# Kernel optimization log

Hardware: AMD Instinct MI355X
Metric: run time of the kernel (lower is better)

The kernel has to match this reference:

```python
import jax, jax.numpy as jnp
from jax import lax
import numpy as np

N, E = 64, 126            # nodes per graph, directed edges (N = E//2 + 1)
BS, T = 32, 512           # batch, train_seq_len
G = BS * T                # total graphs
IN = N * 2                # encoder input_size
H8 = 128 * 8              # hidden_size * 8
OUT = 128                 # output_size (decoder GRU hidden)
L = 2                     # num_layers


def setup_inputs() -> dict:
    key = jax.random.key(0)
    ks = iter(jax.random.split(key, 64))
    def rn(shape, s=0.05):
        return jax.random.normal(next(ks), shape, dtype=jnp.float32) * s
    inp = {}
    inp['x'] = rn((G, N, 2), 1.0)
    inp['edge_index'] = jax.random.randint(next(ks), (2, E), 0, N)
    # GCN params (GCNConv(2,4), GCNConv(4,2), classifier Linear(2,2))
    inp['gcn_w1'] = rn((2, 4), 0.5); inp['gcn_b1'] = rn((4,))
    inp['gcn_w2'] = rn((4, 2), 0.5); inp['gcn_b2'] = rn((2,))
    inp['gcn_cw'] = rn((2, 2), 0.5); inp['gcn_cb'] = rn((2,))
    # Encoder: fl Linear(IN, H8); GRU(H8, H8, L)
    inp['enc_fl_w'] = rn((IN, H8)); inp['enc_fl_b'] = rn((H8,))
    inp['enc_wih'] = rn((L, 3 * H8, H8)); inp['enc_whh'] = rn((L, 3 * H8, H8))
    inp['enc_bih'] = rn((L, 3 * H8)); inp['enc_bhh'] = rn((L, 3 * H8))
    # Decoder: fl Linear(H8, H8); GRU(H8, OUT, L); Linear(OUT, OUT)
    inp['dec_fl_w'] = rn((H8, H8)); inp['dec_fl_b'] = rn((H8,))
    inp['dec_wih0'] = rn((3 * OUT, H8)); inp['dec_wih1'] = rn((3 * OUT, OUT))
    inp['dec_whh'] = rn((L, 3 * OUT, OUT))
    inp['dec_bih'] = rn((L, 3 * OUT)); inp['dec_bhh'] = rn((L, 3 * OUT))
    inp['dec_lin_w'] = rn((OUT, OUT)); inp['dec_lin_b'] = rn((OUT,))
    return inp


def _gcn_conv(h, src, dst, W, b):
    # PyG GCNConv: self-loops + symmetric normalization. h: [G, N, Fin]
    hw = h @ W                                   # [G, N, Fout]
    deg = jnp.ones((N,), hw.dtype).at[dst].add(jnp.ones((E,), hw.dtype))
    dinv = lax.rsqrt(deg)
    norm = dinv[src] * dinv[dst]                 # [E]
    msgs = hw[:, src, :] * norm[None, :, None]   # gather + scale
    agg = jnp.zeros_like(hw).at[:, dst, :].add(msgs)
    agg = agg + hw * (dinv * dinv)[None, :, None]  # self-loop term (norm = 1/deg)
    return agg + b


def _gru_layer(x_seq, wih, whh, bih, bhh):
    # x_seq: [B, T, D]; torch nn.GRU math, h0 = 0
    B = x_seq.shape[0]
    H = whh.shape[1]
    h0 = jnp.zeros((B, H), x_seq.dtype)
    def step(h, x_t):
        gi = x_t @ wih.T + bih
        gh = h @ whh.T + bhh
        i_r, i_z, i_n = jnp.split(gi, 3, axis=-1)
        h_r, h_z, h_n = jnp.split(gh, 3, axis=-1)
        r = jax.nn.sigmoid(i_r + h_r)
        z = jax.nn.sigmoid(i_z + h_z)
        n = jnp.tanh(i_n + r * h_n)
        h_new = (1.0 - z) * n + z * h
        return h_new, h_new
    _, ys = lax.scan(step, h0, jnp.swapaxes(x_seq, 0, 1))
    return jnp.swapaxes(ys, 0, 1)


def reference(x, edge_index, gcn_w1, gcn_b1, gcn_w2, gcn_b2, gcn_cw, gcn_cb,
              enc_fl_w, enc_fl_b, enc_wih, enc_whh, enc_bih, enc_bhh,
              dec_fl_w, dec_fl_b, dec_wih0, dec_wih1, dec_whh, dec_bih, dec_bhh,
              dec_lin_w, dec_lin_b):
    src, dst = edge_index[0], edge_index[1]
    # GCN over all G graphs at once (vectorizes the per-graph Python loop)
    h = jnp.tanh(_gcn_conv(x, src, dst, gcn_w1, gcn_b1))
    h = jnp.tanh(_gcn_conv(h, src, dst, gcn_w2, gcn_b2))
    h = h @ gcn_cw + gcn_cb                      # [G, N, 2]
    res = h.reshape(BS, T, IN)
    # Encoder
    out = jax.nn.relu(res @ enc_fl_w + enc_fl_b)
    for l in range(L):
        out = _gru_layer(out, enc_wih[l], enc_whh[l], enc_bih[l], enc_bhh[l])
    # Decoder (dropout in eval mode = identity)
    d = jax.nn.relu(out @ dec_fl_w + dec_fl_b)
    d = _gru_layer(d, dec_wih0, dec_whh[0], dec_bih[0], dec_bhh[0])
    d = _gru_layer(d, dec_wih1, dec_whh[1], dec_bih[1], dec_bhh[1])
    return d @ dec_lin_w + dec_lin_b             # [BS, T, OUT]
```

## Files before the change

kernel.cpp:

```cpp
#include <hip/hip_runtime.h>

typedef unsigned short u16;
typedef unsigned long long u64;
typedef __attribute__((ext_vector_type(8))) short bf16x8;
typedef __attribute__((ext_vector_type(4))) float f32x4;

#define BSZ 32
#define TT 512
#define GG (BSZ*TT)
#define NNODE 64
#define EE 126
#define H8 1024
#define H3 3072
#define NWAVE 128

__device__ __forceinline__ float b2f(u16 u){
  union { unsigned i; float f; } v; v.i = ((unsigned)u) << 16; return v.f;
}
__device__ __forceinline__ u16 f2b(float f){
  unsigned i = __float_as_uint(f);
  unsigned r = (i + 0x7FFFu + ((i >> 16) & 1u)) >> 16;
  return (u16)r;
}
__device__ __forceinline__ float sigm(float x){ return 1.f/(1.f+__expf(-x)); }
__device__ __forceinline__ float tanh_f(float x){
  float xc = fminf(fmaxf(x, -15.f), 15.f);
  float e = __expf(2.f*xc);
  return (e-1.f)/(e+1.f);
}
__device__ __forceinline__ int prow(int m, int perm){
  return perm ? ((m & (TT-1))*BSZ + (m >> 9)) : m;
}

__global__ __launch_bounds__(256) void detect_dtype(const void* xraw, int* flag){
  __shared__ int cnt;
  if (threadIdx.x == 0) cnt = 0;
  __syncthreads();
  const u16* p = (const u16*)xraw;
  u16 u = p[2*threadIdx.x];
  int e = (u >> 7) & 0xFF;
  int weird = (e < 100 || e > 134) ? 1 : 0;
  atomicAdd(&cnt, weird);
  __syncthreads();
  if (threadIdx.x == 0) *flag = (cnt > 128) ? 1 : 0;
}

__global__ __launch_bounds__(256) void cvt_bf16(const void* __restrict__ in,
                                                u16* __restrict__ out, int n,
                                                const int* __restrict__ flag){
  int i = blockIdx.x*256 + threadIdx.x;
  if (i >= n) return;
  if (*flag) out[i] = f2b(((const float*)in)[i]);
  else       out[i] = ((const u16*)in)[i];
}

__global__ __launch_bounds__(64) void gcn_kernel(
    const u16* __restrict__ x, const int* __restrict__ ei,
    const u16* __restrict__ w1, const u16* __restrict__ b1,
    const u16* __restrict__ w2, const u16* __restrict__ b2,
    const u16* __restrict__ cw, const u16* __restrict__ cb,
    u16* __restrict__ res)
{
  __shared__ int se[EE], de[EE];
  __shared__ float dinv[NNODE];
  __shared__ float nrm[EE];
  __shared__ float hs[NNODE][4];
  const int n = threadIdx.x;
  const int g = blockIdx.x;
  for (int e = n; e < EE; e += 64){ se[e] = ei[e]; de[e] = ei[EE + e]; }
  __syncthreads();
  int cnt = 0;
  for (int e = 0; e < EE; e++) cnt += (de[e] == n) ? 1 : 0;
  float di = rsqrtf(1.0f + (float)cnt);
  dinv[n] = di;
  float x0 = b2f(x[((size_t)g*NNODE + n)*2 + 0]);
  float x1 = b2f(x[((size_t)g*NNODE + n)*2 + 1]);
  float hw[4];
  #pragma unroll
  for (int c = 0; c < 4; c++) hw[c] = x0*b2f(w1[c]) + x1*b2f(w1[4+c]);
  #pragma unroll
  for (int c = 0; c < 4; c++) hs[n][c] = hw[c];
  __syncthreads();
  for (int e = n; e < EE; e += 64) nrm[e] = dinv[se[e]] * dinv[de[e]];
  __syncthreads();
  float selfc = di*di;
  float agg[4];
  #pragma unroll
  for (int c = 0; c < 4; c++) agg[c] = hw[c]*selfc;
  for (int e = 0; e < EE; e++){
    if (de[e] == n){
      float w = nrm[e]; int s = se[e];
      #pragma unroll
      for (int c = 0; c < 4; c++) agg[c] += hs[s][c]*w;
    }
  }
  float h1[4];
  #pragma unroll
  for (int c = 0; c < 4; c++) h1[c] = tanh_f(agg[c] + b2f(b1[c]));
  __syncthreads();
  float hw2[2];
  #pragma unroll
  for (int c = 0; c < 2; c++){
    float s = 0.f;
    #pragma unroll
    for (int k = 0; k < 4; k++) s += h1[k]*b2f(w2[k*2+c]);
    hw2[c] = s;
    hs[n][c] = s;
  }
  __syncthreads();
  float agg2[2] = { hw2[0]*selfc, hw2[1]*selfc };
  for (int e = 0; e < EE; e++){
    if (de[e] == n){
      float w = nrm[e]; int s = se[e];
      agg2[0] += hs[s][0]*w;
      agg2[1] += hs[s][1]*w;
    }
  }
  float h2a = tanh_f(agg2[0] + b2f(b2[0]));
  float h2b = tanh_f(agg2[1] + b2f(b2[1]));
  #pragma unroll
  for (int c = 0; c < 2; c++){
    float o = h2a*b2f(cw[c]) + h2b*b2f(cw[2+c]) + b2f(cb[c]);
    res[(size_t)g*128 + n*2 + c] = f2b(o);
  }
}

__global__ __launch_bounds__(256) void transpose_bf16(
    const u16* __restrict__ in, u16* __restrict__ out, int R, int C)
{
  __shared__ u16 tile[32][33];
  int c0 = blockIdx.x*32, r0 = blockIdx.y*32;
  for (int i = threadIdx.y; i < 32; i += 8)
    tile[i][threadIdx.x] = in[(size_t)(r0+i)*C + c0 + threadIdx.x];
  __syncthreads();
  for (int i = threadIdx.y; i < 32; i += 8)
    out[(size_t)(c0+i)*R + r0 + threadIdx.x] = tile[threadIdx.x][i];
}

__global__ __launch_bounds__(256) void gemm_nt(
    const u16* __restrict__ A, const u16* __restrict__ Bm,
    const u16* __restrict__ bias, void* __restrict__ C,
    int M, int N, int K, int relu, int permA, int permC,
    const int* __restrict__ outflag)
{
  const int wave = threadIdx.x >> 6;
  const int lane = threadIdx.x & 63;
  const int wm = wave >> 1, wn = wave & 1;
  const int q = lane >> 4, lr = lane & 15;
  const int mBase = blockIdx.y*128 + wm*64;
  const int nBase = blockIdx.x*128 + wn*64;
  f32x4 acc[4][4] = {};
  const u16* ap[4]; const u16* bp[4];
  #pragma unroll
  for (int i = 0; i < 4; i++){
    ap[i] = A + (size_t)prow(mBase + i*16 + lr, permA)*K + q*8;
    bp[i] = Bm + (size_t)(nBase + i*16 + lr)*K + q*8;
  }
  for (int kb = 0; kb < K; kb += 32){
    bf16x8 av[4], bv[4];
    #pragma unroll
    for (int i = 0; i < 4; i++){
      av[i] = *(const bf16x8*)ap[i]; bv[i] = *(const bf16x8*)bp[i];
      ap[i] += 32; bp[i] += 32;
    }
    #pragma unroll
    for (int mi = 0; mi < 4; mi++)
      #pragma unroll
      for (int ni = 0; ni < 4; ni++)
        acc[mi][ni] = __builtin_amdgcn_mfma_f32_16x16x32_bf16(av[mi], bv[ni], acc[mi][ni], 0, 0, 0);
  }
  const int of32 = outflag ? *outflag : 0;
  #pragma unroll
  for (int ni = 0; ni < 4; ni++){
    int col = nBase + ni*16 + lr;
    float bb = bias ? b2f(bias[col]) : 0.f;
    #pragma unroll
    for (int mi = 0; mi < 4; mi++){
      #pragma unroll
      for (int r = 0; r < 4; r++){
        int row = prow(mBase + mi*16 + q*4 + r, permC);
        float v = acc[mi][ni][r] + bb;
        if (relu) v = fmaxf(v, 0.f);
        size_t idx = (size_t)row*N + col;
        if (of32) ((float*)C)[idx] = v;
        else      ((u16*)C)[idx]   = f2b(v);
      }
    }
  }
}

__global__ __launch_bounds__(64) void enc_rec(
    const u16* __restrict__ gi,
    const u16* __restrict__ whh,
    const u16* __restrict__ bhh,
    u16* __restrict__ seq,
    int* __restrict__ cnt)
{
  const int wg = blockIdx.x;
  const int lane = threadIdx.x & 63;
  const int q = lane >> 4, lr = lane & 15;
  const int j = (wg >> 1)*16 + lr;
  const int bbase = (wg & 1)*16;
  const int sub = wg & 7;
  const float bh_r = b2f(bhh[j]);
  const float bh_z = b2f(bhh[H8 + j]);
  const float bh_n = b2f(bhh[2*H8 + j]);
  const u16* wp0 = whh + (size_t)(0*H8 + j)*H8 + q*8;
  const u16* wp1 = whh + (size_t)(1*H8 + j)*H8 + q*8;
  const u16* wp2 = whh + (size_t)(2*H8 + j)*H8 + q*8;
  float hreg[4] = {0.f,0.f,0.f,0.f};
  u16 gpre[12];
  #pragma unroll
  for (int r = 0; r < 4; r++){
    size_t row = (size_t)(bbase + q*4 + r)*H3;
    gpre[r]   = gi[row + j];
    gpre[4+r] = gi[row + H8 + j];
    gpre[8+r] = gi[row + 2*H8 + j];
  }
  for (int t = 0; t < TT; t++){
    if (t > 0){
      for (;;){
        int s = 0;
        #pragma unroll
        for (int i = 0; i < 8; i++)
          s += __hip_atomic_load(&cnt[i*TT + (t-1)], __ATOMIC_RELAXED, __HIP_MEMORY_SCOPE_AGENT);
        if (s == NWAVE) break;
        __builtin_amdgcn_s_sleep(1);
      }
      asm volatile("" ::: "memory");
    }
    float gr_[4], gz_[4], gn_[4];
    #pragma unroll
    for (int r = 0; r < 4; r++){
      gr_[r] = b2f(gpre[r]); gz_[r] = b2f(gpre[4+r]); gn_[r] = b2f(gpre[8+r]);
    }
    f32x4 acc0 = {}, acc1 = {}, acc2 = {};
    if (t > 0){
      const u16* ap = seq + (size_t)((t-1)*BSZ + bbase + lr)*H8 + q*8;
      #pragma unroll 8
      for (int kb = 0; kb < 32; kb++){
        const u64* p = (const u64*)(ap + kb*32);
        u64 lo = __hip_atomic_load(p,     __ATOMIC_RELAXED, __HIP_MEMORY_SCOPE_AGENT);
        u64 hi = __hip_atomic_load(p + 1, __ATOMIC_RELAXED, __HIP_MEMORY_SCOPE_AGENT);
        union { u64 v[2]; bf16x8 b; } a; a.v[0] = lo; a.v[1] = hi;
        bf16x8 w0 = *(const bf16x8*)(wp0 + kb*32);
        bf16x8 w1 = *(const bf16x8*)(wp1 + kb*32);
        bf16x8 w2 = *(const bf16x8*)(wp2 + kb*32);
        acc0 = __builtin_amdgcn_mfma_f32_16x16x32_bf16(a.b, w0, acc0, 0,0,0);
        acc1 = __builtin_amdgcn_mfma_f32_16x16x32_bf16(a.b, w1, acc1, 0,0,0);
        acc2 = __builtin_amdgcn_mfma_f32_16x16x32_bf16(a.b, w2, acc2, 0,0,0);
      }
    }
    #pragma unroll
    for (int r = 0; r < 4; r++){
      float rr = sigm(gr_[r] + acc0[r] + bh_r);
      float zz = sigm(gz_[r] + acc1[r] + bh_z);
      float nn = tanh_f(gn_[r] + rr*(acc2[r] + bh_n));
      float hnew = (1.f - zz)*nn + zz*hreg[r];
      hreg[r] = hnew;
      __hip_atomic_store(&seq[(size_t)(t*BSZ + bbase + q*4 + r)*H8 + j], f2b(hnew),
                         __ATOMIC_RELAXED, __HIP_MEMORY_SCOPE_AGENT);
    }
    asm volatile("s_waitcnt vmcnt(0)" ::: "memory");
    if (lane == 0)
      __hip_atomic_fetch_add(&cnt[sub*TT + t], 1, __ATOMIC_RELAXED, __HIP_MEMORY_SCOPE_AGENT);
    if (t + 1 < TT){
      #pragma unroll
      for (int r = 0; r < 4; r++){
        size_t row = (size_t)((t+1)*BSZ + bbase + q*4 + r)*H3;
        gpre[r]   = gi[row + j];
        gpre[4+r] = gi[row + H8 + j];
        gpre[8+r] = gi[row + 2*H8 + j];
      }
    }
  }
}

__global__ __launch_bounds__(256) void dec_rec(
    const u16* __restrict__ gi,
    const u16* __restrict__ whh,
    const u16* __restrict__ bhh,
    u16* __restrict__ seq)
{
  __shared__ u16 hlds[16*136];
  const int bb = blockIdx.x*16;
  const int tid = threadIdx.x;
  const int w = tid >> 6, lane = tid & 63, q = lane >> 4, lr = lane & 15;
  bf16x8 wreg[3][2][4];
  #pragma unroll
  for (int g2 = 0; g2 < 3; g2++)
    #pragma unroll
    for (int nt = 0; nt < 2; nt++){
      int jj = g2*128 + w*32 + nt*16 + lr;
      #pragma unroll
      for (int kb = 0; kb < 4; kb++)
        wreg[g2][nt][kb] = *(const bf16x8*)(whh + (size_t)jj*128 + kb*32 + q*8);
    }
  float bh[3][2];
  #pragma unroll
  for (int g2 = 0; g2 < 3; g2++)
    #pragma unroll
    for (int nt = 0; nt < 2; nt++)
      bh[g2][nt] = b2f(bhh[g2*128 + w*32 + nt*16 + lr]);
  float hreg[2][4] = {};
  u16 gpre[3][2][4];
  #pragma unroll
  for (int r = 0; r < 4; r++){
    size_t row = (size_t)(bb + q*4 + r)*384;
    #pragma unroll
    for (int nt = 0; nt < 2; nt++){
      int jj = w*32 + nt*16 + lr;
      #pragma unroll
      for (int g2 = 0; g2 < 3; g2++)
        gpre[g2][nt][r] = gi[row + g2*128 + jj];
    }
  }
  __syncthreads();
  for (int t = 0; t < TT; t++){
    float gif[3][2][4];
    #pragma unroll
    for (int g2 = 0; g2 < 3; g2++)
      #pragma unroll
      for (int nt = 0; nt < 2; nt++)
        #pragma unroll
        for (int r = 0; r < 4; r++)
          gif[g2][nt][r] = b2f(gpre[g2][nt][r]);
    f32x4 acc[3][2] = {};
    if (t > 0){
      #pragma unroll
      for (int kb = 0; kb < 4; kb++){
        bf16x8 a = *(const bf16x8*)(hlds + lr*136 + kb*32 + q*8);
        #pragma unroll
        for (int g2 = 0; g2 < 3; g2++)
          #pragma unroll
          for (int nt = 0; nt < 2; nt++)
            acc[g2][nt] = __builtin_amdgcn_mfma_f32_16x16x32_bf16(a, wreg[g2][nt][kb], acc[g2][nt], 0,0,0);
      }
    }
    __syncthreads();
    #pragma unroll
    for (int nt = 0; nt < 2; nt++)
      #pragma unroll
      for (int r = 0; r < 4; r++){
        int jj = w*32 + nt*16 + lr;
        int b = bb + q*4 + r;
        float rr = sigm(gif[0][nt][r] + acc[0][nt][r] + bh[0][nt]);
        float zz = sigm(gif[1][nt][r] + acc[1][nt][r] + bh[1][nt]);
        float nn = tanh_f(gif[2][nt][r] + rr*(acc[2][nt][r] + bh[2][nt]));
        float hnew = (1.f - zz)*nn + zz*hreg[nt][r];
        hreg[nt][r] = hnew;
        u16 hb = f2b(hnew);
        hlds[(q*4 + r)*136 + jj] = hb;
        seq[(size_t)(t*BSZ + b)*128 + jj] = hb;
      }
    if (t + 1 < TT){
      #pragma unroll
      for (int r = 0; r < 4; r++){
        size_t row = (size_t)((t+1)*BSZ + bb + q*4 + r)*384;
        #pragma unroll
        for (int nt = 0; nt < 2; nt++){
          int jj = w*32 + nt*16 + lr;
          #pragma unroll
          for (int g2 = 0; g2 < 3; g2++)
            gpre[g2][nt][r] = gi[row + g2*128 + jj];
        }
      }
    }
    __syncthreads();
  }
}

extern "C" void kernel_launch(void* const* d_in, const int* in_sizes, int n_in,
                              void* d_out, int out_size, void* d_ws, size_t ws_size,
                              hipStream_t stream)
{
  const void* x    = d_in[0];
  const int* ei    = (const int*)d_in[1];

  const size_t NEED = (size_t)164 << 20;
  if (ws_size < NEED) return;
  char* wsb = (char*)d_ws;
  const size_t KB = 1024, MB = 1024*1024;

  int* syncv = (int*)wsb;
  int* flag  = (int*)(wsb + 40*KB);
  u16* gw1_c  = (u16*)(wsb + 1*MB + 0);
  u16* gb1_c  = (u16*)(wsb + 1*MB + 64);
  u16* gw2_c  = (u16*)(wsb + 1*MB + 128);
  u16* gb2_c  = (u16*)(wsb + 1*MB + 192);
  u16* gcw_c  = (u16*)(wsb + 1*MB + 256);
  u16* gcb_c  = (u16*)(wsb + 1*MB + 320);
  u16* efb_c  = (u16*)(wsb + 1*MB + 4*KB);
  u16* ebih_c = (u16*)(wsb + 1*MB + 8*KB);
  u16* ebhh_c = (u16*)(wsb + 1*MB + 24*KB);
  u16* dfb_c  = (u16*)(wsb + 1*MB + 40*KB);
  u16* dbih_c = (u16*)(wsb + 1*MB + 45*KB);
  u16* dbhh_c = (u16*)(wsb + 1*MB + 47*KB);
  u16* dlb_c  = (u16*)(wsb + 1*MB + 49*KB);
  u16* wT3    = (u16*)(wsb + 1*MB + 64*KB);
  u16* dlw_c  = (u16*)(wsb + 1*MB + 128*KB);
  u16* efw_c  = (u16*)(wsb + 1*MB + 192*KB);
  u16* wT1    = (u16*)(wsb + 1*MB + 448*KB);
  u16* dfw_c  = (u16*)(wsb + 2*MB);
  u16* wT2    = (u16*)(wsb + 4*MB);
  u16* dwih0_c= (u16*)(wsb + 6*MB);
  u16* dwih1_c= (u16*)(wsb + 7*MB);
  u16* dwhh_c = (u16*)(wsb + 7*MB + 128*KB);
  u16* ewih_c = (u16*)(wsb + 8*MB);
  u16* ewhh_c = (u16*)(wsb + 20*MB);
  u16* res    = (u16*)(wsb + 32*MB);
  u16* bufA   = (u16*)(wsb + 36*MB);
  u16* bufC   = (u16*)(wsb + 68*MB);
  u16* x_c    = bufC;
  u16* giD    = (u16*)(wsb + 100*MB);

  hipMemsetAsync(syncv, 0, 32*KB, stream);
  detect_dtype<<<1, 256, 0, stream>>>(x, flag);

  auto cvt = [&](int idx, u16* dst, int n){
    cvt_bf16<<<(n + 255)/256, 256, 0, stream>>>(d_in[idx], dst, n, flag);
  };
  cvt(0,  x_c,     GG*NNODE*2);
  cvt(2,  gw1_c, 8);  cvt(3, gb1_c, 4);  cvt(4, gw2_c, 8);
  cvt(5,  gb2_c, 2);  cvt(6, gcw_c, 4);  cvt(7, gcb_c, 2);
  cvt(8,  efw_c,   128*1024);   cvt(9,  efb_c, 1024);
  cvt(10, ewih_c,  2*3072*1024);
  cvt(11, ewhh_c,  2*3072*1024);
  cvt(12, ebih_c,  2*3072);     cvt(13, ebhh_c, 2*3072);
  cvt(14, dfw_c,   1024*1024);  cvt(15, dfb_c, 1024);
  cvt(16, dwih0_c, 384*1024);   cvt(17, dwih1_c, 384*128);
  cvt(18, dwhh_c,  2*384*128);
  cvt(19, dbih_c,  2*384);      cvt(20, dbhh_c, 2*384);
  cvt(21, dlw_c,   128*128);    cvt(22, dlb_c, 128);

  transpose_bf16<<<dim3(1024/32, 128/32),  dim3(32,8), 0, stream>>>(efw_c, wT1, 128, 1024);
  transpose_bf16<<<dim3(1024/32, 1024/32), dim3(32,8), 0, stream>>>(dfw_c, wT2, 1024, 1024);
  transpose_bf16<<<dim3(128/32, 128/32),   dim3(32,8), 0, stream>>>(dlw_c, wT3, 128, 128);

  gcn_kernel<<<GG, 64, 0, stream>>>(x_c, ei, gw1_c, gb1_c, gw2_c, gb2_c, gcw_c, gcb_c, res);

  gemm_nt<<<dim3(1024/128, GG/128), 256, 0, stream>>>(res, wT1, efb_c, bufA, GG, 1024, 128, 1, 0, 1, nullptr);
  gemm_nt<<<dim3(3072/128, GG/128), 256, 0, stream>>>(bufA, ewih_c, ebih_c, bufC, GG, 3072, 1024, 0, 1, 1, nullptr);
  enc_rec<<<NWAVE, 64, 0, stream>>>(bufC, ewhh_c, ebhh_c, bufA, syncv);
  gemm_nt<<<dim3(3072/128, GG/128), 256, 0, stream>>>(bufA, ewih_c + 3072*1024, ebih_c + 3072, bufC, GG, 3072, 1024, 0, 1, 1, nullptr);
  enc_rec<<<NWAVE, 64, 0, stream>>>(bufC, ewhh_c + 3072*1024, ebhh_c + 3072, bufA, syncv + 8*TT);

  u16* d0 = bufC;
  gemm_nt<<<dim3(1024/128, GG/128), 256, 0, stream>>>(bufA, wT2, dfb_c, d0, GG, 1024, 1024, 1, 1, 1, nullptr);
  gemm_nt<<<dim3(384/128, GG/128), 256, 0, stream>>>(d0, dwih0_c, dbih_c, giD, GG, 384, 1024, 0, 1, 1, nullptr);
  dec_rec<<<2, 256, 0, stream>>>(giD, dwhh_c, dbhh_c, res);
  gemm_nt<<<dim3(384/128, GG/128), 256, 0, stream>>>(res, dwih1_c, dbih_c + 384, giD, GG, 384, 128, 0, 1, 1, nullptr);
  dec_rec<<<2, 256, 0, stream>>>(giD, dwhh_c + 384*128, dbhh_c + 384, bufA);

  gemm_nt<<<dim3(128/128, GG/128), 256, 0, stream>>>(bufA, wT3, dlb_c, d_out, GG, 128, 128, 0, 1, 0, flag);
}
```

Before: 12.47 ms.

## Wavefront-pipeline encoder GRU layers and fuse decoder layers with output linear

Runs both encoder GRU layers in one persistent kernel, with layer 1 one step behind layer 0. Layer 1 computes its input projection on the fly from the layer-0 state instead of a separate full-sequence GEMM, and both layers share a global-counter barrier. The decoder's two GRU layers and the final linear are fused into one 512-thread block pipeline that uses double-buffered LDS states and prefetches the gate inputs. This removes two recurrent launches, one large GEMM and the serialized layer-1 time chain. In exchange, layer-1 waves do more per-step work, namely the input matmul streamed from global weights each step, and twice as many waves contend on the spin barrier.

```diff
diff --git a/kernel.cpp b/kernel.cpp
--- a/kernel.cpp
+++ b/kernel.cpp
@@ -12,7 +12,7 @@
 #define EE 126
 #define H8 1024
 #define H3 3072
-#define NWAVE 128
+#define NARRIVE 256
 
 __device__ __forceinline__ float b2f(u16 u){
   union { unsigned i; float f; } v; v.i = ((unsigned)u) << 16; return v.f;
@@ -30,6 +30,9 @@
 }
 __device__ __forceinline__ int prow(int m, int perm){
   return perm ? ((m & (TT-1))*BSZ + (m >> 9)) : m;
+}
+__device__ __forceinline__ u64 aload64(const u64* p){
+  return __hip_atomic_load(p, __ATOMIC_RELAXED, __HIP_MEMORY_SCOPE_AGENT);
 }
 
 __global__ __launch_bounds__(256) void detect_dtype(const void* xraw, int* flag){
@@ -139,9 +142,8 @@
 
 __global__ __launch_bounds__(256) void gemm_nt(
     const u16* __restrict__ A, const u16* __restrict__ Bm,
-    const u16* __restrict__ bias, void* __restrict__ C,
-    int M, int N, int K, int relu, int permA, int permC,
-    const int* __restrict__ outflag)
+    const u16* __restrict__ bias, u16* __restrict__ C,
+    int M, int N, int K, int relu, int permA, int permC)
 {
   const int wave = threadIdx.x >> 6;
   const int lane = threadIdx.x & 63;
@@ -169,7 +171,6 @@
       for (int ni = 0; ni < 4; ni++)
         acc[mi][ni] = __builtin_amdgcn_mfma_f32_16x16x32_bf16(av[mi], bv[ni], acc[mi][ni], 0, 0, 0);
   }
-  const int of32 = outflag ? *outflag : 0;
   #pragma unroll
   for (int ni = 0; ni < 4; ni++){
     int col = nBase + ni*16 + lr;
@@ -181,192 +182,337 @@
         int row = prow(mBase + mi*16 + q*4 + r, permC);
         float v = acc[mi][ni][r] + bb;
         if (relu) v = fmaxf(v, 0.f);
-        size_t idx = (size_t)row*N + col;
-        if (of32) ((float*)C)[idx] = v;
-        else      ((u16*)C)[idx]   = f2b(v);
+        C[(size_t)row*N + col] = f2b(v);
       }
     }
   }
 }
 
-__global__ __launch_bounds__(64) void enc_rec(
-    const u16* __restrict__ gi,
-    const u16* __restrict__ whh,
-    const u16* __restrict__ bhh,
-    u16* __restrict__ seq,
-    int* __restrict__ cnt)
+__device__ __forceinline__ void spinwait(int* cnt, int r){
+  for (;;){
+    int s = 0;
+    #pragma unroll
+    for (int i = 0; i < 8; i++)
+      s += __hip_atomic_load(&cnt[i*(TT+1) + r], __ATOMIC_RELAXED, __HIP_MEMORY_SCOPE_AGENT);
+    if (s == NARRIVE) break;
+    __builtin_amdgcn_s_sleep(1);
+  }
+  asm volatile("" ::: "memory");
+}
+
+__global__ __launch_bounds__(64) void enc_fused(
+    const u16* gi,
+    const u16* wih1,
+    const u16* whh0, const u16* whh1,
+    const u16* bih1, const u16* bhh0, const u16* bhh1,
+    u16* h0seq,
+    u16* h1seq,
+    int* cnt)
 {
-  const int wg = blockIdx.x;
+  const int wid = blockIdx.x;
+  const int stage = wid >> 7;
+  const int wid2 = wid & 127;
   const int lane = threadIdx.x & 63;
   const int q = lane >> 4, lr = lane & 15;
-  const int j = (wg >> 1)*16 + lr;
-  const int bbase = (wg & 1)*16;
-  const int sub = wg & 7;
-  const float bh_r = b2f(bhh[j]);
-  const float bh_z = b2f(bhh[H8 + j]);
-  const float bh_n = b2f(bhh[2*H8 + j]);
-  const u16* wp0 = whh + (size_t)(0*H8 + j)*H8 + q*8;
-  const u16* wp1 = whh + (size_t)(1*H8 + j)*H8 + q*8;
-  const u16* wp2 = whh + (size_t)(2*H8 + j)*H8 + q*8;
+  const int jg = wid2 >> 1, bh = wid2 & 1;
+  const int j = jg*16 + lr;
+  const int bbase = bh*16;
+  const int sub = wid & 7;
   float hreg[4] = {0.f,0.f,0.f,0.f};
-  u16 gpre[12];
-  #pragma unroll
-  for (int r = 0; r < 4; r++){
-    size_t row = (size_t)(bbase + q*4 + r)*H3;
-    gpre[r]   = gi[row + j];
-    gpre[4+r] = gi[row + H8 + j];
-    gpre[8+r] = gi[row + 2*H8 + j];
-  }
-  for (int t = 0; t < TT; t++){
-    if (t > 0){
-      for (;;){
-        int s = 0;
-        #pragma unroll
-        for (int i = 0; i < 8; i++)
-          s += __hip_atomic_load(&cnt[i*TT + (t-1)], __ATOMIC_RELAXED, __HIP_MEMORY_SCOPE_AGENT);
-        if (s == NWAVE) break;
-        __builtin_amdgcn_s_sleep(1);
+
+  if (stage == 0){
+    const float bh_r = b2f(bhh0[j]);
+    const float bh_z = b2f(bhh0[H8 + j]);
+    const float bh_n = b2f(bhh0[2*H8 + j]);
+    const u16* wp0 = whh0 + (size_t)(0*H8 + j)*H8 + q*8;
+    const u16* wp1 = whh0 + (size_t)(1*H8 + j)*H8 + q*8;
+    const u16* wp2 = whh0 + (size_t)(2*H8 + j)*H8 + q*8;
+    u16 gpre[12];
+    #pragma unroll
+    for (int r = 0; r < 4; r++){
+      size_t row = (size_t)(bbase + q*4 + r)*H3;
+      gpre[r]   = gi[row + j];
+      gpre[4+r] = gi[row + H8 + j];
+      gpre[8+r] = gi[row + 2*H8 + j];
+    }
+    for (int rd = 0; rd <= TT; rd++){
+      if (rd > 0) spinwait(cnt, rd - 1);
+      if (rd < TT){
+        const int t = rd;
+        float gr_[4], gz_[4], gn_[4];
+        #pragma unroll
+        for (int r = 0; r < 4; r++){
+          gr_[r] = b2f(gpre[r]); gz_[r] = b2f(gpre[4+r]); gn_[r] = b2f(gpre[8+r]);
+        }
+        f32x4 acc0 = {}, acc1 = {}, acc2 = {};
+        if (t > 0){
+          const u16* ap = h0seq + (size_t)((t-1)*BSZ + bbase + lr)*H8 + q*8;
+          #pragma unroll 8
+          for (int kb = 0; kb < 32; kb++){
+            const u64* p = (const u64*)(ap + kb*32);
+            union { u64 v[2]; bf16x8 b; } A; A.v[0] = aload64(p); A.v[1] = aload64(p+1);
+            bf16x8 w0 = *(const bf16x8*)(wp0 + kb*32);
+            bf16x8 w1 = *(const bf16x8*)(wp1 + kb*32);
+            bf16x8 w2 = *(const bf16x8*)(wp2 + kb*32);
+            acc0 = __builtin_amdgcn_mfma_f32_16x16x32_bf16(A.b, w0, acc0, 0,0,0);
+            acc1 = __builtin_amdgcn_mfma_f32_16x16x32_bf16(A.b, w1, acc1, 0,0,0);
+            acc2 = __builtin_amdgcn_mfma_f32_16x16x32_bf16(A.b, w2, acc2, 0,0,0);
+          }
+        }
+        #pragma unroll
+        for (int r = 0; r < 4; r++){
+          float rr = sigm(gr_[r] + acc0[r] + bh_r);
+          float zz = sigm(gz_[r] + acc1[r] + bh_z);
+          float nn = tanh_f(gn_[r] + rr*(acc2[r] + bh_n));
+          float hnew = (1.f - zz)*nn + zz*hreg[r];
+          hreg[r] = hnew;
+          __hip_atomic_store(&h0seq[(size_t)(t*BSZ + bbase + q*4 + r)*H8 + j], f2b(hnew),
+                             __ATOMIC_RELAXED, __HIP_MEMORY_SCOPE_AGENT);
+        }
       }
-      asm volatile("" ::: "memory");
-    }
-    float gr_[4], gz_[4], gn_[4];
-    #pragma unroll
-    for (int r = 0; r < 4; r++){
-      gr_[r] = b2f(gpre[r]); gz_[r] = b2f(gpre[4+r]); gn_[r] = b2f(gpre[8+r]);
-    }
-    f32x4 acc0 = {}, acc1 = {}, acc2 = {};
-    if (t > 0){
-      const u16* ap = seq + (size_t)((t-1)*BSZ + bbase + lr)*H8 + q*8;
-      #pragma unroll 8
-      for (int kb = 0; kb < 32; kb++){
-        const u64* p = (const u64*)(ap + kb*32);
-        u64 lo = __hip_atomic_load(p,     __ATOMIC_RELAXED, __HIP_MEMORY_SCOPE_AGENT);
-        u64 hi = __hip_atomic_load(p + 1, __ATOMIC_RELAXED, __HIP_MEMORY_SCOPE_AGENT);
-        union { u64 v[2]; bf16x8 b; } a; a.v[0] = lo; a.v[1] = hi;
-        bf16x8 w0 = *(const bf16x8*)(wp0 + kb*32);
-        bf16x8 w1 = *(const bf16x8*)(wp1 + kb*32);
-        bf16x8 w2 = *(const bf16x8*)(wp2 + kb*32);
-        acc0 = __builtin_amdgcn_mfma_f32_16x16x32_bf16(a.b, w0, acc0, 0,0,0);
-        acc1 = __builtin_amdgcn_mfma_f32_16x16x32_bf16(a.b, w1, acc1, 0,0,0);
-        acc2 = __builtin_amdgcn_mfma_f32_16x16x32_bf16(a.b, w2, acc2, 0,0,0);
+      asm volatile("s_waitcnt vmcnt(0)" ::: "memory");
+      if (lane == 0)
+        __hip_atomic_fetch_add(&cnt[sub*(TT+1) + rd], 1, __ATOMIC_RELAXED, __HIP_MEMORY_SCOPE_AGENT);
+      if (rd + 1 < TT){
+        #pragma unroll
+        for (int r = 0; r < 4; r++){
+          size_t row = (size_t)((rd+1)*BSZ + bbase + q*4 + r)*H3;
+          gpre[r]   = gi[row + j];
+          gpre[4+r] = gi[row + H8 + j];
+          gpre[8+r] = gi[row + 2*H8 + j];
+        }
       }
     }
-    #pragma unroll
-    for (int r = 0; r < 4; r++){
-      float rr = sigm(gr_[r] + acc0[r] + bh_r);
-      float zz = sigm(gz_[r] + acc1[r] + bh_z);
-      float nn = tanh_f(gn_[r] + rr*(acc2[r] + bh_n));
-      float hnew = (1.f - zz)*nn + zz*hreg[r];
-      hreg[r] = hnew;
-      __hip_atomic_store(&seq[(size_t)(t*BSZ + bbase + q*4 + r)*H8 + j], f2b(hnew),
-                         __ATOMIC_RELAXED, __HIP_MEMORY_SCOPE_AGENT);
-    }
-    asm volatile("s_waitcnt vmcnt(0)" ::: "memory");
-    if (lane == 0)
-      __hip_atomic_fetch_add(&cnt[sub*TT + t], 1, __ATOMIC_RELAXED, __HIP_MEMORY_SCOPE_AGENT);
-    if (t + 1 < TT){
-      #pragma unroll
-      for (int r = 0; r < 4; r++){
-        size_t row = (size_t)((t+1)*BSZ + bbase + q*4 + r)*H3;
-        gpre[r]   = gi[row + j];
-        gpre[4+r] = gi[row + H8 + j];
-        gpre[8+r] = gi[row + 2*H8 + j];
+  } else {
+    const float bir = b2f(bih1[j]);
+    const float biz = b2f(bih1[H8 + j]);
+    const float bin = b2f(bih1[2*H8 + j]);
+    const float bhr = b2f(bhh1[j]);
+    const float bhz = b2f(bhh1[H8 + j]);
+    const float bhn = b2f(bhh1[2*H8 + j]);
+    const u16* ip0 = wih1 + (size_t)(0*H8 + j)*H8 + q*8;
+    const u16* ip1 = wih1 + (size_t)(1*H8 + j)*H8 + q*8;
+    const u16* ip2 = wih1 + (size_t)(2*H8 + j)*H8 + q*8;
+    const u16* hp0 = whh1 + (size_t)(0*H8 + j)*H8 + q*8;
+    const u16* hp1 = whh1 + (size_t)(1*H8 + j)*H8 + q*8;
+    const u16* hp2 = whh1 + (size_t)(2*H8 + j)*H8 + q*8;
+    for (int rd = 0; rd <= TT; rd++){
+      if (rd > 0) spinwait(cnt, rd - 1);
+      if (rd >= 1){
+        const int t = rd - 1;
+        f32x4 aI0 = {}, aI1 = {}, aI2 = {}, aH0 = {}, aH1 = {}, aH2 = {};
+        const u16* a0p = h0seq + (size_t)(t*BSZ + bbase + lr)*H8 + q*8;
+        if (t > 0){
+          const u16* a1p = h1seq + (size_t)((t-1)*BSZ + bbase + lr)*H8 + q*8;
+          #pragma unroll 4
+          for (int kb = 0; kb < 32; kb++){
+            const u64* p0 = (const u64*)(a0p + kb*32);
+            union { u64 v[2]; bf16x8 b; } A0; A0.v[0] = aload64(p0); A0.v[1] = aload64(p0+1);
+            const u64* p1 = (const u64*)(a1p + kb*32);
+            union { u64 v[2]; bf16x8 b; } A1; A1.v[0] = aload64(p1); A1.v[1] = aload64(p1+1);
+            bf16x8 i0 = *(const bf16x8*)(ip0 + kb*32);
+            bf16x8 i1 = *(const bf16x8*)(ip1 + kb*32);
+            bf16x8 i2 = *(const bf16x8*)(ip2 + kb*32);
+            bf16x8 h0v = *(const bf16x8*)(hp0 + kb*32);
+            bf16x8 h1v = *(const bf16x8*)(hp1 + kb*32);
+            bf16x8 h2v = *(const bf16x8*)(hp2 + kb*32);
+            aI0 = __builtin_amdgcn_mfma_f32_16x16x32_bf16(A0.b, i0, aI0, 0,0,0);
+            aI1 = __builtin_amdgcn_mfma_f32_16x16x32_bf16(A0.b, i1, aI1, 0,0,0);
+            aI2 = __builtin_amdgcn_mfma_f32_16x16x32_bf16(A0.b, i2, aI2, 0,0,0);
+            aH0 = __builtin_amdgcn_mfma_f32_16x16x32_bf16(A1.b, h0v, aH0, 0,0,0);
+            aH1 = __builtin_amdgcn_mfma_f32_16x16x32_bf16(A1.b, h1v, aH1, 0,0,0);
+            aH2 = __builtin_amdgcn_mfma_f32_16x16x32_bf16(A1.b, h2v, aH2, 0,0,0);
+          }
+        } else {
+          #pragma unroll 8
+          for (int kb = 0; kb < 32; kb++){
+            const u64* p0 = (const u64*)(a0p + kb*32);
+            union { u64 v[2]; bf16x8 b; } A0; A0.v[0] = aload64(p0); A0.v[1] = aload64(p0+1);
+            bf16x8 i0 = *(const bf16x8*)(ip0 + kb*32);
+            bf16x8 i1 = *(const bf16x8*)(ip1 + kb*32);
+            bf16x8 i2 = *(const bf16x8*)(ip2 + kb*32);
+            aI0 = __builtin_amdgcn_mfma_f32_16x16x32_bf16(A0.b, i0, aI0, 0,0,0);
+            aI1 = __builtin_amdgcn_mfma_f32_16x16x32_bf16(A0.b, i1, aI1, 0,0,0);
+            aI2 = __builtin_amdgcn_mfma_f32_16x16x32_bf16(A0.b, i2, aI2, 0,0,0);
+          }
+        }
+        #pragma unroll
+        for (int r = 0; r < 4; r++){
+          float rr = sigm(aI0[r] + bir + aH0[r] + bhr);
+          float zz = sigm(aI1[r] + biz + aH1[r] + bhz);
+          float nn = tanh_f(aI2[r] + bin + rr*(aH2[r] + bhn));
+          float hnew = (1.f - zz)*nn + zz*hreg[r];
+          hreg[r] = hnew;
+          __hip_atomic_store(&h1seq[(size_t)(t*BSZ + bbase + q*4 + r)*H8 + j], f2b(hnew),
+                             __ATOMIC_RELAXED, __HIP_MEMORY_SCOPE_AGENT);
+        }
       }
-    }
-  }
-}
-
-__global__ __launch_bounds__(256) void dec_rec(
-    const u16* __restrict__ gi,
-    const u16* __restrict__ whh,
-    const u16* __restrict__ bhh,
-    u16* __restrict__ seq)
+      asm volatile("s_waitcnt vmcnt(0)" ::: "memory");
+      if (lane == 0)
+        __hip_atomic_fetch_add(&cnt[sub*(TT+1) + rd], 1, __ATOMIC_RELAXED, __HIP_MEMORY_SCOPE_AGENT);
+    }
+  }
+}
+
+__global__ __launch_bounds__(512) void dec_fused(
+    const u16* __restrict__ gi0,
+    const u16* __restrict__ whh0, const u16* __restrict__ bhh0,
+    const u16* __restrict__ wih1, const u16* __restrict__ whh1,
+    const u16* __restrict__ bih1, const u16* __restrict__ bhh1,
+    const u16* __restrict__ dlwT, const u16* __restrict__ dlb,
+    void* __restrict__ out, const int* __restrict__ flag)
 {
-  __shared__ u16 hlds[16*136];
+  __shared__ u16 h3[2][16*136];
+  __shared__ u16 h4[2][16*136];
+  __shared__ u16 gib[2][6144];
   const int bb = blockIdx.x*16;
   const int tid = threadIdx.x;
-  const int w = tid >> 6, lane = tid & 63, q = lane >> 4, lr = lane & 15;
-  bf16x8 wreg[3][2][4];
+  const int wv = tid >> 6, lane = tid & 63, q = lane >> 4, lr = lane & 15;
+  const int stage = wv >> 2, w = wv & 3;
+  const int of32 = *flag;
+  float hreg[2][4] = {};
+  float b0[3][2], bi1[3][2], bh1[3][2], bl[2];
+  bf16x8 lw[2][4];
   #pragma unroll
   for (int g2 = 0; g2 < 3; g2++)
     #pragma unroll
     for (int nt = 0; nt < 2; nt++){
       int jj = g2*128 + w*32 + nt*16 + lr;
+      if (stage == 0) b0[g2][nt] = b2f(bhh0[jj]);
+      else { bi1[g2][nt] = b2f(bih1[jj]); bh1[g2][nt] = b2f(bhh1[jj]); }
+    }
+  if (stage == 1){
+    #pragma unroll
+    for (int nt = 0; nt < 2; nt++){
+      int jj = w*32 + nt*16 + lr;
+      bl[nt] = b2f(dlb[jj]);
       #pragma unroll
       for (int kb = 0; kb < 4; kb++)
-        wreg[g2][nt][kb] = *(const bf16x8*)(whh + (size_t)jj*128 + kb*32 + q*8);
-    }
-  float bh[3][2];
-  #pragma unroll
-  for (int g2 = 0; g2 < 3; g2++)
-    #pragma unroll
-    for (int nt = 0; nt < 2; nt++)
-      bh[g2][nt] = b2f(bhh[g2*128 + w*32 + nt*16 + lr]);
-  float hreg[2][4] = {};
-  u16 gpre[3][2][4];
-  #pragma unroll
-  for (int r = 0; r < 4; r++){
-    size_t row = (size_t)(bb + q*4 + r)*384;
-    #pragma unroll
-    for (int nt = 0; nt < 2; nt++){
-      int jj = w*32 + nt*16 + lr;
-      #pragma unroll
-      for (int g2 = 0; g2 < 3; g2++)
-        gpre[g2][nt][r] = gi[row + g2*128 + jj];
-    }
-  }
-  __syncthreads();
-  for (int t = 0; t < TT; t++){
-    float gif[3][2][4];
-    #pragma unroll
-    for (int g2 = 0; g2 < 3; g2++)
-      #pragma unroll
-      for (int nt = 0; nt < 2; nt++)
-        #pragma unroll
-        for (int r = 0; r < 4; r++)
-          gif[g2][nt][r] = b2f(gpre[g2][nt][r]);
-    f32x4 acc[3][2] = {};
-    if (t > 0){
-      #pragma unroll
-      for (int kb = 0; kb < 4; kb++){
-        bf16x8 a = *(const bf16x8*)(hlds + lr*136 + kb*32 + q*8);
-        #pragma unroll
-        for (int g2 = 0; g2 < 3; g2++)
+        lw[nt][kb] = *(const bf16x8*)(dlwT + (size_t)jj*128 + kb*32 + q*8);
+    }
+  }
+  {
+    const u16* gb = gi0 + (size_t)bb*384;
+    bf16x8 g0 = *(const bf16x8*)(gb + tid*8);
+    *(bf16x8*)(gib[0] + tid*8) = g0;
+    if (tid < 256){
+      bf16x8 g1 = *(const bf16x8*)(gb + (512+tid)*8);
+      *(bf16x8*)(gib[0] + (512+tid)*8) = g1;
+    }
+  }
+  for (int rd = 0; rd < TT+2; rd++){
+    __syncthreads();
+    bf16x8 g0, g1;
+    const int stg = (rd + 1 < TT);
+    if (stg){
+      const u16* gb = gi0 + (size_t)((rd+1)*BSZ + bb)*384;
+      g0 = *(const bf16x8*)(gb + tid*8);
+      if (tid < 256) g1 = *(const bf16x8*)(gb + (512+tid)*8);
+    }
+    if (stage == 0){
+      if (rd < TT){
+        float gif[3][2][4];
+        #pragma unroll
+        for (int r = 0; r < 4; r++){
+          int base = (q*4 + r)*384;
+          #pragma unroll
+          for (int g2 = 0; g2 < 3; g2++)
+            #pragma unroll
+            for (int nt = 0; nt < 2; nt++)
+              gif[g2][nt][r] = b2f(gib[rd&1][base + g2*128 + w*32 + nt*16 + lr]);
+        }
+        f32x4 accH[3][2] = {};
+        if (rd > 0){
+          #pragma unroll
+          for (int kb = 0; kb < 4; kb++){
+            bf16x8 a = *(const bf16x8*)(&h3[(rd-1)&1][lr*136 + kb*32 + q*8]);
+            #pragma unroll
+            for (int g2 = 0; g2 < 3; g2++)
+              #pragma unroll
+              for (int nt = 0; nt < 2; nt++){
+                bf16x8 bw = *(const bf16x8*)(whh0 + (size_t)(g2*128 + w*32 + nt*16 + lr)*128 + kb*32 + q*8);
+                accH[g2][nt] = __builtin_amdgcn_mfma_f32_16x16x32_bf16(a, bw, accH[g2][nt], 0,0,0);
+              }
+          }
+        }
+        #pragma unroll
+        for (int nt = 0; nt < 2; nt++)
+          #pragma unroll
+          for (int r = 0; r < 4; r++){
+            float rr = sigm(gif[0][nt][r] + accH[0][nt][r] + b0[0][nt]);
+            float zz = sigm(gif[1][nt][r] + accH[1][nt][r] + b0[1][nt]);
+            float nn = tanh_f(gif[2][nt][r] + rr*(accH[2][nt][r] + b0[2][nt]));
+            float hnew = (1.f - zz)*nn + zz*hreg[nt][r];
+            hreg[nt][r] = hnew;
+            h3[rd&1][(q*4 + r)*136 + w*32 + nt*16 + lr] = f2b(hnew);
+          }
+      }
+    } else {
+      if (rd >= 1 && rd <= TT){
+        const int t1 = rd - 1;
+        f32x4 accI[3][2] = {}, accH[3][2] = {};
+        #pragma unroll
+        for (int kb = 0; kb < 4; kb++){
+          bf16x8 a0 = *(const bf16x8*)(&h3[(rd-1)&1][lr*136 + kb*32 + q*8]);
+          #pragma unroll
+          for (int g2 = 0; g2 < 3; g2++)
+            #pragma unroll
+            for (int nt = 0; nt < 2; nt++){
+              bf16x8 bw = *(const bf16x8*)(wih1 + (size_t)(g2*128 + w*32 + nt*16 + lr)*128 + kb*32 + q*8);
+              accI[g2][nt] = __builtin_amdgcn_mfma_f32_16x16x32_bf16(a0, bw, accI[g2][nt], 0,0,0);
+            }
+        }
+        if (t1 > 0){
+          #pragma unroll
+          for (int kb = 0; kb < 4; kb++){
+            bf16x8 a1 = *(const bf16x8*)(&h4[(rd-2)&1][lr*136 + kb*32 + q*8]);
+            #pragma unroll
+            for (int g2 = 0; g2 < 3; g2++)
+              #pragma unroll
+              for (int nt = 0; nt < 2; nt++){
+                bf16x8 bw = *(const bf16x8*)(whh1 + (size_t)(g2*128 + w*32 + nt*16 + lr)*128 + kb*32 + q*8);
+                accH[g2][nt] = __builtin_amdgcn_mfma_f32_16x16x32_bf16(a1, bw, accH[g2][nt], 0,0,0);
+              }
+          }
+        }
+        #pragma unroll
+        for (int nt = 0; nt < 2; nt++)
+          #pragma unroll
+          for (int r = 0; r < 4; r++){
+            float rr = sigm(accI[0][nt][r] + bi1[0][nt] + accH[0][nt][r] + bh1[0][nt]);
+            float zz = sigm(accI[1][nt][r] + bi1[1][nt] + accH[1][nt][r] + bh1[1][nt]);
+            float nn = tanh_f(accI[2][nt][r] + bi1[2][nt] + rr*(accH[2][nt][r] + bh1[2][nt]));
+            float hnew = (1.f - zz)*nn + zz*hreg[nt][r];
+            hreg[nt][r] = hnew;
+            h4[(rd-1)&1][(q*4 + r)*136 + w*32 + nt*16 + lr] = f2b(hnew);
+          }
+      }
+      if (rd >= 2){
+        const int tf = rd - 2;
+        f32x4 accF[2] = {};
+        #pragma unroll
+        for (int kb = 0; kb < 4; kb++){
+          bf16x8 a = *(const bf16x8*)(&h4[(rd-2)&1][lr*136 + kb*32 + q*8]);
           #pragma unroll
           for (int nt = 0; nt < 2; nt++)
-            acc[g2][nt] = __builtin_amdgcn_mfma_f32_16x16x32_bf16(a, wreg[g2][nt][kb], acc[g2][nt], 0,0,0);
+            accF[nt] = __builtin_amdgcn_mfma_f32_16x16x32_bf16(a, lw[nt][kb], accF[nt], 0,0,0);
+        }
+        #pragma unroll
+        for (int nt = 0; nt < 2; nt++)
+          #pragma unroll
+          for (int r = 0; r < 4; r++){
+            float v = accF[nt][r] + bl[nt];
+            int b = bb + q*4 + r;
+            size_t idx = (size_t)(b*TT + tf)*128 + w*32 + nt*16 + lr;
+            if (of32) ((float*)out)[idx] = v;
+            else      ((u16*)out)[idx]   = f2b(v);
+          }
       }
     }
-    __syncthreads();
-    #pragma unroll
-    for (int nt = 0; nt < 2; nt++)
-      #pragma unroll
-      for (int r = 0; r < 4; r++){
-        int jj = w*32 + nt*16 + lr;
-        int b = bb + q*4 + r;
-        float rr = sigm(gif[0][nt][r] + acc[0][nt][r] + bh[0][nt]);
-        float zz = sigm(gif[1][nt][r] + acc[1][nt][r] + bh[1][nt]);
-        float nn = tanh_f(gif[2][nt][r] + rr*(acc[2][nt][r] + bh[2][nt]));
-        float hnew = (1.f - zz)*nn + zz*hreg[nt][r];
-        hreg[nt][r] = hnew;
-        u16 hb = f2b(hnew);
-        hlds[(q*4 + r)*136 + jj] = hb;
-        seq[(size_t)(t*BSZ + b)*128 + jj] = hb;
-      }
-    if (t + 1 < TT){
-      #pragma unroll
-      for (int r = 0; r < 4; r++){
-        size_t row = (size_t)((t+1)*BSZ + bb + q*4 + r)*384;
-        #pragma unroll
-        for (int nt = 0; nt < 2; nt++){
-          int jj = w*32 + nt*16 + lr;
-          #pragma unroll
-          for (int g2 = 0; g2 < 3; g2++)
-            gpre[g2][nt][r] = gi[row + g2*128 + jj];
-        }
-      }
-    }
-    __syncthreads();
+    if (stg){
+      *(bf16x8*)(gib[(rd+1)&1] + tid*8) = g0;
+      if (tid < 256) *(bf16x8*)(gib[(rd+1)&1] + (512+tid)*8) = g1;
+    }
   }
 }
 
@@ -412,7 +558,9 @@
   u16* bufA   = (u16*)(wsb + 36*MB);
   u16* bufC   = (u16*)(wsb + 68*MB);
   u16* x_c    = bufC;
-  u16* giD    = (u16*)(wsb + 100*MB);
+  u16* h1seq  = bufC;
+  u16* d0     = (u16*)(wsb + 100*MB);
+  u16* giD0   = bufA;
 
   hipMemsetAsync(syncv, 0, 32*KB, stream);
   detect_dtype<<<1, 256, 0, stream>>>(x, flag);
@@ -439,18 +587,14 @@
 
   gcn_kernel<<<GG, 64, 0, stream>>>(x_c, ei, gw1_c, gb1_c, gw2_c, gb2_c, gcw_c, gcb_c, res);
 
-  gemm_nt<<<dim3(1024/128, GG/128), 256, 0, stream>>>(res, wT1, efb_c, bufA, GG, 1024, 128, 1, 0, 1, nullptr);
-  gemm_nt<<<dim3(3072/128, GG/128), 256, 0, stream>>>(bufA, ewih_c, ebih_c, bufC, GG, 3072, 1024, 0, 1, 1, nullptr);
-  enc_rec<<<NWAVE, 64, 0, stream>>>(bufC, ewhh_c, ebhh_c, bufA, syncv);
-  gemm_nt<<<dim3(3072/128, GG/128), 256, 0, stream>>>(bufA, ewih_c + 3072*1024, ebih_c + 3072, bufC, GG, 3072, 1024, 0, 1, 1, nullptr);
-  enc_rec<<<NWAVE, 64, 0, stream>>>(bufC, ewhh_c + 3072*1024, ebhh_c + 3072, bufA, syncv + 8*TT);
-
-  u16* d0 = bufC;
-  gemm_nt<<<dim3(1024/128, GG/128), 256, 0, stream>>>(bufA, wT2, dfb_c, d0, GG, 1024, 1024, 1, 1, 1, nullptr);
-  gemm_nt<<<dim3(384/128, GG/128), 256, 0, stream>>>(d0, dwih0_c, dbih_c, giD, GG, 384, 1024, 0, 1, 1, nullptr);
-  dec_rec<<<2, 256, 0, stream>>>(giD, dwhh_c, dbhh_c, res);
-  gemm_nt<<<dim3(384/128, GG/128), 256, 0, stream>>>(res, dwih1_c, dbih_c + 384, giD, GG, 384, 128, 0, 1, 1, nullptr);
-  dec_rec<<<2, 256, 0, stream>>>(giD, dwhh_c + 384*128, dbhh_c + 384, bufA);
-
-  gemm_nt<<<dim3(128/128, GG/128), 256, 0, stream>>>(bufA, wT3, dlb_c, d_out, GG, 128, 128, 0, 1, 0, flag);
-}
+  gemm_nt<<<dim3(1024/128, GG/128), 256, 0, stream>>>(res, wT1, efb_c, bufA, GG, 1024, 128, 1, 0, 1);
+  gemm_nt<<<dim3(3072/128, GG/128), 256, 0, stream>>>(bufA, ewih_c, ebih_c, bufC, GG, 3072, 1024, 0, 1, 1);
+  enc_fused<<<256, 64, 0, stream>>>(bufC, ewih_c + 3072*1024, ewhh_c, ewhh_c + 3072*1024,
+                                    ebih_c + 3072, ebhh_c, ebhh_c + 3072,
+                                    bufA, h1seq, syncv);
+
+  gemm_nt<<<dim3(1024/128, GG/128), 256, 0, stream>>>(h1seq, wT2, dfb_c, d0, GG, 1024, 1024, 1, 1, 1);
+  gemm_nt<<<dim3(384/128, GG/128), 256, 0, stream>>>(d0, dwih0_c, dbih_c, giD0, GG, 384, 1024, 0, 1, 1);
+  dec_fused<<<2, 512, 0, stream>>>(giD0, dwhh_c, dbhh_c, dwih1_c, dwhh_c + 384*128,
+                                   dbih_c + 384, dbhh_c + 384, wT3, dlb_c, d_out, flag);
+}
```

After: 17.48 ms. 40.2% more time.

## Restructure encoder GRU recurrence into 32 four-wave blocks with LDS-staged hidden state

Applied to the files above, without the earlier changes.

The encoder recurrent kernel now runs as 32 workgroups of 4 waves instead of 128 single-wave workgroups. Each step, one thread spins on fewer cross-block counters, then the block cooperatively copies the full previous hidden state into shared memory before the MFMA loop. This cuts the number of global atomic arrivals and polls per timestep and replaces scattered global loads of the hidden state with LDS reads. In exchange it adds two block barriers per step and a 64KB shared-memory copy on the critical path.

```diff
diff --git a/kernel.cpp b/kernel.cpp
--- a/kernel.cpp
+++ b/kernel.cpp
@@ -12,7 +12,7 @@
 #define EE 126
 #define H8 1024
 #define H3 3072
-#define NWAVE 128
+#define NWG2 32
 
 __device__ __forceinline__ float b2f(u16 u){
   union { unsigned i; float f; } v; v.i = ((unsigned)u) << 16; return v.f;
@@ -30,6 +30,9 @@
 }
 __device__ __forceinline__ int prow(int m, int perm){
   return perm ? ((m & (TT-1))*BSZ + (m >> 9)) : m;
+}
+__device__ __forceinline__ u64 aload64(const u64* p){
+  return __hip_atomic_load(p, __ATOMIC_RELAXED, __HIP_MEMORY_SCOPE_AGENT);
 }
 
 __global__ __launch_bounds__(256) void detect_dtype(const void* xraw, int* flag){
@@ -189,19 +192,20 @@
   }
 }
 
-__global__ __launch_bounds__(64) void enc_rec(
+__global__ __launch_bounds__(256) void enc_rec2(
     const u16* __restrict__ gi,
     const u16* __restrict__ whh,
     const u16* __restrict__ bhh,
     u16* __restrict__ seq,
     int* __restrict__ cnt)
 {
+  __shared__ u16 hbuf[32*1032];
   const int wg = blockIdx.x;
-  const int lane = threadIdx.x & 63;
-  const int q = lane >> 4, lr = lane & 15;
-  const int j = (wg >> 1)*16 + lr;
-  const int bbase = (wg & 1)*16;
-  const int sub = wg & 7;
+  const int tid = threadIdx.x;
+  const int w = tid >> 6, lane = tid & 63, q = lane >> 4, lr = lane & 15;
+  const int jt = w >> 1, bh2 = w & 1;
+  const int j = wg*32 + jt*16 + lr;
+  const int bbase = bh2*16;
   const float bh_r = b2f(bhh[j]);
   const float bh_z = b2f(bhh[H8 + j]);
   const float bh_n = b2f(bhh[2*H8 + j]);
@@ -218,17 +222,6 @@
     gpre[8+r] = gi[row + 2*H8 + j];
   }
   for (int t = 0; t < TT; t++){
-    if (t > 0){
-      for (;;){
-        int s = 0;
-        #pragma unroll
-        for (int i = 0; i < 8; i++)
-          s += __hip_atomic_load(&cnt[i*TT + (t-1)], __ATOMIC_RELAXED, __HIP_MEMORY_SCOPE_AGENT);
-        if (s == NWAVE) break;
-        __builtin_amdgcn_s_sleep(1);
-      }
-      asm volatile("" ::: "memory");
-    }
     float gr_[4], gz_[4], gn_[4];
     #pragma unroll
     for (int r = 0; r < 4; r++){
@@ -236,19 +229,16 @@
     }
     f32x4 acc0 = {}, acc1 = {}, acc2 = {};
     if (t > 0){
-      const u16* ap = seq + (size_t)((t-1)*BSZ + bbase + lr)*H8 + q*8;
+      const u16* abase = hbuf + (size_t)(bbase + lr)*1032 + q*8;
       #pragma unroll 8
       for (int kb = 0; kb < 32; kb++){
-        const u64* p = (const u64*)(ap + kb*32);
-        u64 lo = __hip_atomic_load(p,     __ATOMIC_RELAXED, __HIP_MEMORY_SCOPE_AGENT);
-        u64 hi = __hip_atomic_load(p + 1, __ATOMIC_RELAXED, __HIP_MEMORY_SCOPE_AGENT);
-        union { u64 v[2]; bf16x8 b; } a; a.v[0] = lo; a.v[1] = hi;
+        bf16x8 a  = *(const bf16x8*)(abase + kb*32);
         bf16x8 w0 = *(const bf16x8*)(wp0 + kb*32);
         bf16x8 w1 = *(const bf16x8*)(wp1 + kb*32);
         bf16x8 w2 = *(const bf16x8*)(wp2 + kb*32);
-        acc0 = __builtin_amdgcn_mfma_f32_16x16x32_bf16(a.b, w0, acc0, 0,0,0);
-        acc1 = __builtin_amdgcn_mfma_f32_16x16x32_bf16(a.b, w1, acc1, 0,0,0);
-        acc2 = __builtin_amdgcn_mfma_f32_16x16x32_bf16(a.b, w2, acc2, 0,0,0);
+        acc0 = __builtin_amdgcn_mfma_f32_16x16x32_bf16(a, w0, acc0, 0,0,0);
+        acc1 = __builtin_amdgcn_mfma_f32_16x16x32_bf16(a, w1, acc1, 0,0,0);
+        acc2 = __builtin_amdgcn_mfma_f32_16x16x32_bf16(a, w2, acc2, 0,0,0);
       }
     }
     #pragma unroll
@@ -262,8 +252,9 @@
                          __ATOMIC_RELAXED, __HIP_MEMORY_SCOPE_AGENT);
     }
     asm volatile("s_waitcnt vmcnt(0)" ::: "memory");
-    if (lane == 0)
-      __hip_atomic_fetch_add(&cnt[sub*TT + t], 1, __ATOMIC_RELAXED, __HIP_MEMORY_SCOPE_AGENT);
+    __syncthreads();
+    if (tid == 0)
+      __hip_atomic_fetch_add(&cnt[(wg & 3)*TT + t], 1, __ATOMIC_RELAXED, __HIP_MEMORY_SCOPE_AGENT);
     if (t + 1 < TT){
       #pragma unroll
       for (int r = 0; r < 4; r++){
@@ -272,6 +263,28 @@
         gpre[4+r] = gi[row + H8 + j];
         gpre[8+r] = gi[row + 2*H8 + j];
       }
+      if (tid == 0){
+        for (;;){
+          int s = 0;
+          #pragma unroll
+          for (int i = 0; i < 4; i++)
+            s += __hip_atomic_load(&cnt[i*TT + t], __ATOMIC_RELAXED, __HIP_MEMORY_SCOPE_AGENT);
+          if (s == NWG2) break;
+          __builtin_amdgcn_s_sleep(1);
+        }
+      }
+      __syncthreads();
+      const u64* src = (const u64*)(seq + (size_t)t*BSZ*H8);
+      #pragma unroll
+      for (int i = 0; i < 16; i++){
+        int c = i*256 + tid;
+        int b = c >> 7, kc = c & 127;
+        u64 lo = aload64(src + (size_t)b*256 + kc*2);
+        u64 hi = aload64(src + (size_t)b*256 + kc*2 + 1);
+        u64* dst = (u64*)(hbuf + (size_t)b*1032 + kc*8);
+        dst[0] = lo; dst[1] = hi;
+      }
+      __syncthreads();
     }
   }
 }
@@ -383,7 +396,7 @@
   const size_t KB = 1024, MB = 1024*1024;
 
   int* syncv = (int*)wsb;
-  int* flag  = (int*)(wsb + 40*KB);
+  int* flag  = (int*)(wsb + 24*KB);
   u16* gw1_c  = (u16*)(wsb + 1*MB + 0);
   u16* gb1_c  = (u16*)(wsb + 1*MB + 64);
   u16* gw2_c  = (u16*)(wsb + 1*MB + 128);
@@ -414,7 +427,7 @@
   u16* x_c    = bufC;
   u16* giD    = (u16*)(wsb + 100*MB);
 
-  hipMemsetAsync(syncv, 0, 32*KB, stream);
+  hipMemsetAsync(syncv, 0, 16*KB, stream);
   detect_dtype<<<1, 256, 0, stream>>>(x, flag);
 
   auto cvt = [&](int idx, u16* dst, int n){
@@ -441,9 +454,9 @@
 
   gemm_nt<<<dim3(1024/128, GG/128), 256, 0, stream>>>(res, wT1, efb_c, bufA, GG, 1024, 128, 1, 0, 1, nullptr);
   gemm_nt<<<dim3(3072/128, GG/128), 256, 0, stream>>>(bufA, ewih_c, ebih_c, bufC, GG, 3072, 1024, 0, 1, 1, nullptr);
-  enc_rec<<<NWAVE, 64, 0, stream>>>(bufC, ewhh_c, ebhh_c, bufA, syncv);
+  enc_rec2<<<NWG2, 256, 0, stream>>>(bufC, ewhh_c, ebhh_c, bufA, syncv);
   gemm_nt<<<dim3(3072/128, GG/128), 256, 0, stream>>>(bufA, ewih_c + 3072*1024, ebih_c + 3072, bufC, GG, 3072, 1024, 0, 1, 1, nullptr);
-  enc_rec<<<NWAVE, 64, 0, stream>>>(bufC, ewhh_c + 3072*1024, ebhh_c + 3072, bufA, syncv + 8*TT);
+  enc_rec2<<<NWG2, 256, 0, stream>>>(bufC, ewhh_c + 3072*1024, ebhh_c + 3072, bufA, syncv + 4*TT);
 
   u16* d0 = bufC;
   gemm_nt<<<dim3(1024/128, GG/128), 256, 0, stream>>>(bufA, wT2, dfb_c, d0, GG, 1024, 1024, 1, 1, 1, nullptr);
```

Result: slower. 19.38 ms (+55.5%).
